# Performance work log

Measured on AMD Instinct MI355X. Metric: run time of the kernel, lower is better.

## Reference

```python
import jax, jax.numpy as jnp
import numpy as np

N_NODES = 50000
N_EDGES = 800000
HIDDEN = 128
HEADS = 8
HEAD_DIM = HIDDEN // HEADS
N_REL = 64
SCALE = np.sqrt(HEAD_DIM).astype(np.float32)


def setup_inputs() -> dict:
    key = jax.random.key(0)
    ks = jax.random.split(key, 12)
    s = 1.0 / np.sqrt(2 * HIDDEN)
    s2 = 1.0 / np.sqrt(HIDDEN)
    return {
        "node_features": jax.random.normal(ks[0], (N_NODES, HIDDEN), jnp.float32),
        "query_embedding": jax.random.normal(ks[1], (1, HIDDEN), jnp.float32),
        "relation_embeddings": jax.random.normal(ks[2], (N_REL, HIDDEN), jnp.float32),
        "Wq": jax.random.uniform(ks[3], (2 * HIDDEN, HIDDEN), jnp.float32, -s, s),
        "bq": jnp.zeros((HIDDEN,), jnp.float32),
        "Wk": jax.random.uniform(ks[4], (2 * HIDDEN, HIDDEN), jnp.float32, -s, s),
        "bk": jnp.zeros((HIDDEN,), jnp.float32),
        "Wv": jax.random.uniform(ks[5], (HIDDEN, HIDDEN), jnp.float32, -s2, s2),
        "bv": jnp.zeros((HIDDEN,), jnp.float32),
        "Wo": jax.random.uniform(ks[6], (HIDDEN, HIDDEN), jnp.float32, -s2, s2),
        "bo": jnp.zeros((HIDDEN,), jnp.float32),
        "edge_index": jax.random.randint(ks[7], (2, N_EDGES), 0, N_NODES, jnp.int64),
        "edge_type": jax.random.randint(ks[8], (N_EDGES,), 0, N_REL, jnp.int64),
    }


def reference(node_features, query_embedding, relation_embeddings,
              Wq, bq, Wk, bk, Wv, bv, Wo, bo, edge_index, edge_type):
    n = node_features.shape[0]
    # expand query to all nodes and concat: [N, 2*hidden]
    q_exp = jnp.broadcast_to(query_embedding, (n, HIDDEN))
    nq = jnp.concatenate([node_features, q_exp], axis=-1)
    q = (nq @ Wq + bq).reshape(n, HEADS, HEAD_DIM)
    k = (nq @ Wk + bk).reshape(n, HEADS, HEAD_DIM)
    v = (node_features @ Wv + bv).reshape(n, HEADS, HEAD_DIM)

    src, dst = edge_index[0], edge_index[1]
    rel_bias = relation_embeddings[edge_type].reshape(-1, HEADS, HEAD_DIM)

    # edge-wise scores [E, heads]
    scores = jnp.sum(q[dst] * (k[src] + rel_bias), axis=-1) / SCALE

    # sparse softmax grouped by dst; torch init of max buffer is 0 -> clamp at 0
    seg_max = jax.ops.segment_max(scores, dst, num_segments=n)
    seg_max = jnp.maximum(seg_max, 0.0)
    exp_s = jnp.exp(scores - seg_max[dst])
    seg_sum = jax.ops.segment_sum(exp_s, dst, num_segments=n)
    attn = exp_s / (seg_sum[dst] + 1e-8)  # [E, heads]

    messages = attn[:, :, None] * v[src]  # [E, heads, head_dim]
    out = jax.ops.segment_sum(messages, dst, num_segments=n)  # [N, heads, head_dim]
    out = out.reshape(n, HIDDEN)
    return out @ Wo + bo
```

## Files before the change

### kernel.cpp

```cpp
#include <hip/hip_runtime.h>
#include <math.h>

#define N_NODES 50000
#define N_EDGES 800000
#define HID 128
#define HEADS 8
#define HDIM 16
#define NBIN 196
#define CAPB 5120
#define K2_BLOCKS 196
#define K2_EPT 16
#define QKV_BLOCKS 782
#define NFB_BLOCKS 3125

typedef __attribute__((ext_vector_type(8))) short short8;
typedef __attribute__((ext_vector_type(4))) float floatx4;

#if defined(__has_builtin)
#if __has_builtin(__builtin_amdgcn_fdot2_f32_bf16)
#define HAVE_DOT2 1
#endif
#endif
#ifndef HAVE_DOT2
#define HAVE_DOT2 0
#endif

#if HAVE_DOT2
typedef __attribute__((ext_vector_type(2))) __bf16 bf16x2;
__device__ __forceinline__ float dot2acc(unsigned int a, unsigned int b, float c) {
    return __builtin_amdgcn_fdot2_f32_bf16(__builtin_bit_cast(bf16x2, a),
                                           __builtin_bit_cast(bf16x2, b), c, false);
}
#endif

__device__ __forceinline__ float bf_lo(unsigned int d) { return __uint_as_float(d << 16); }
__device__ __forceinline__ float bf_hi(unsigned int d) { return __uint_as_float(d & 0xFFFF0000u); }
__device__ __forceinline__ unsigned short f2bf(float f) {
    unsigned int u = __float_as_uint(f);
    u = (u + 0x7FFFu + ((u >> 16) & 1u)) >> 16;
    return (unsigned short)u;
}
__device__ __forceinline__ unsigned int pack_bf2(float a, float b) {
    return (unsigned int)f2bf(a) | ((unsigned int)f2bf(b) << 16);
}

__global__ __launch_bounds__(256) void prep_kernel(
    const float* __restrict__ nf,
    const float* __restrict__ query, const float* __restrict__ rel,
    const float* __restrict__ Wq, const float* __restrict__ bq,
    const float* __restrict__ Wk, const float* __restrict__ bk,
    const float* __restrict__ Wv, const float* __restrict__ Wo,
    const int* __restrict__ ei, const int* __restrict__ et,
    int* __restrict__ cursor, unsigned long long* __restrict__ recs,
    unsigned short* __restrict__ Wt, unsigned short* __restrict__ relbf,
    float* __restrict__ bqe, float* __restrict__ bke,
    unsigned short* __restrict__ nfb) {
    int b = blockIdx.x, tid = threadIdx.x;
    if (b < K2_BLOCKS) {
        __shared__ int hist[NBIN];
        __shared__ int base2[NBIN];
        __shared__ int lcur[NBIN];
        for (int i = tid; i < NBIN; i += 256) { hist[i] = 0; lcur[i] = 0; }
        __syncthreads();
        int e0 = b * (256 * K2_EPT);
        unsigned long long rec[K2_EPT];
        int bin[K2_EPT];
        #pragma unroll
        for (int i = 0; i < K2_EPT; ++i) {
            int e = e0 + i * 256 + tid;
            bin[i] = -1;
            if (e < N_EDGES) {
                unsigned int d = (unsigned)ei[N_EDGES + e];
                unsigned int s = (unsigned)ei[e];
                unsigned int t = (unsigned)et[e];
                rec[i] = ((unsigned long long)d << 22) | (t << 16) | s;
                bin[i] = (int)(d >> 8);
                atomicAdd(&hist[bin[i]], 1);
            }
        }
        __syncthreads();
        for (int i = tid; i < NBIN; i += 256) {
            int c = hist[i];
            base2[i] = (c > 0) ? (i * CAPB + atomicAdd(&cursor[i], c)) : 0;
        }
        __syncthreads();
        #pragma unroll
        for (int i = 0; i < K2_EPT; ++i) {
            if (bin[i] >= 0) {
                int pos = atomicAdd(&lcur[bin[i]], 1);
                recs[(size_t)base2[bin[i]] + pos] = rec[i];
            }
        }
        return;
    }
    b -= K2_BLOCKS;
    if (b < NFB_BLOCKS) {
        int base = b * 2048 + tid * 8;
        const float4* p = (const float4*)(nf + base);
        float4 a0 = p[0], a1 = p[1];
        short8 f;
        f[0] = (short)f2bf(a0.x); f[1] = (short)f2bf(a0.y);
        f[2] = (short)f2bf(a0.z); f[3] = (short)f2bf(a0.w);
        f[4] = (short)f2bf(a1.x); f[5] = (short)f2bf(a1.y);
        f[6] = (short)f2bf(a1.z); f[7] = (short)f2bf(a1.w);
        *(short8*)(nfb + base) = f;
        return;
    }
    b -= NFB_BLOCKS;
    if (b < 256) {
        int idx = b * 256 + tid;
        if (idx < 64 * HID) relbf[idx] = f2bf(rel[idx]);
        int m = idx >> 14;
        int rem = idx & 16383;
        int n = rem >> 7, k = rem & 127;
        const float* W = (m == 0) ? Wq : (m == 1) ? Wk : (m == 2) ? Wv : Wo;
        Wt[idx] = f2bf(W[k * HID + n]);
        return;
    }
    {
        __shared__ float fred[256];
        const float* W  = (b == 256) ? Wq : Wk;
        const float* bb = (b == 256) ? bq : bk;
        float* dst      = (b == 256) ? bqe : bke;
        int j = tid & 127;
        int half = tid >> 7;
        float a = 0.0f;
        int i0 = half * 64;
        for (int i = 0; i < 64; ++i) a += query[i0 + i] * W[(HID + i0 + i) * HID + j];
        fred[tid] = a;
        __syncthreads();
        if (half == 0) dst[j] = fred[j] + fred[128 + j] + bb[j];
    }
}

__global__ __launch_bounds__(256) void qkv_kernel(
    const unsigned short* __restrict__ nfb, const unsigned short* __restrict__ Wt,
    const float* __restrict__ bqe, const float* __restrict__ bke, const float* __restrict__ bv,
    const int* __restrict__ cursor, const unsigned long long* __restrict__ recs,
    unsigned int* __restrict__ esort, unsigned int* __restrict__ nodeinfo,
    unsigned short* __restrict__ qb16, unsigned short* __restrict__ kv16) {
    if (blockIdx.x < NBIN) {
        int bkt = blockIdx.x;
        int tid = threadIdx.x;
        __shared__ int hist[256];
        __shared__ int scan[256];
        __shared__ int sbase[256];
        __shared__ int lcur[256];
        hist[tid] = 0; lcur[tid] = 0;
        __syncthreads();
        int cnt = cursor[bkt];
        const unsigned long long* rb = recs + (size_t)bkt * CAPB;
        for (int i = tid; i < cnt; i += 256)
            atomicAdd(&hist[(int)((rb[i] >> 22) & 0xFF)], 1);
        __syncthreads();
        int v = hist[tid];
        scan[tid] = v;
        __syncthreads();
        for (int off = 1; off < 256; off <<= 1) {
            int a = (tid >= off) ? scan[tid - off] : 0;
            __syncthreads();
            scan[tid] += a;
            __syncthreads();
        }
        int excl = scan[tid] - v;
        sbase[tid] = excl;
        int node = bkt * 256 + tid;
        if (node < N_NODES) {
            unsigned int startg = (unsigned)(bkt * CAPB + excl);
            unsigned int deg = (unsigned)(v < 255 ? v : 255);
            nodeinfo[node] = (startg << 8) | deg;
        }
        __syncthreads();
        for (int i = tid; i < cnt; i += 256) {
            unsigned long long r = rb[i];
            int low = (int)((r >> 22) & 0xFF);
            int pos = atomicAdd(&lcur[low], 1);
            esort[(size_t)bkt * CAPB + sbase[low] + pos] = (unsigned int)(r & 0x3FFFFF);
        }
        return;
    }
    int row0 = (blockIdx.x - NBIN) * 64;
    int wave = threadIdx.x >> 6;
    int lane = threadIdx.x & 63;
    int col  = lane & 15;
    int quad = lane >> 4;

    short8 afr[4][4];
    #pragma unroll
    for (int t = 0; t < 4; ++t) {
        int arow = row0 + t * 16 + col;
        int asafe = (arow < N_NODES) ? arow : (N_NODES - 1);
        #pragma unroll
        for (int kk = 0; kk < 4; ++kk)
            afr[t][kk] = *(const short8*)(nfb + (size_t)asafe * HID + kk * 32 + quad * 8);
    }
    const float* biases[3] = {bqe, bke, bv};
    #pragma unroll
    for (int m = 0; m < 3; ++m) {
        const unsigned short* W = Wt + (size_t)m * HID * HID;
        #pragma unroll
        for (int nn = 0; nn < 2; ++nn) {
            int n = wave * 2 + nn;
            float b = biases[m][n * 16 + col];
            floatx4 acc[4];
            #pragma unroll
            for (int t = 0; t < 4; ++t) acc[t] = (floatx4){b, b, b, b};
            short8 bfr[4];
            #pragma unroll
            for (int kk = 0; kk < 4; ++kk)
                bfr[kk] = *(const short8*)(W + (size_t)(n * 16 + col) * HID + kk * 32 + quad * 8);
            #pragma unroll
            for (int kk = 0; kk < 4; ++kk)
                #pragma unroll
                for (int t = 0; t < 4; ++t)
                    acc[t] = __builtin_amdgcn_mfma_f32_16x16x32_bf16(afr[t][kk], bfr[kk], acc[t], 0, 0, 0);
            #pragma unroll
            for (int t = 0; t < 4; ++t) {
                #pragma unroll
                for (int i = 0; i < 4; ++i) {
                    int r = row0 + t * 16 + quad * 4 + i;
                    if (r < N_NODES) {
                        int c = n * 16 + col;
                        if (m == 0)      qb16[(size_t)r * HID + c] = f2bf(acc[t][i]);
                        else if (m == 1) kv16[(size_t)r * 256 + c] = f2bf(acc[t][i]);
                        else             kv16[(size_t)r * 256 + 128 + c] = f2bf(acc[t][i]);
                    }
                }
            }
        }
    }
}

__global__ __launch_bounds__(256) void attn_kernel(
    const unsigned int* __restrict__ qb, const unsigned int* __restrict__ kvu,
    const unsigned int* __restrict__ relu,
    const unsigned int* __restrict__ nodeinfo, const unsigned int* __restrict__ esort,
    unsigned int* __restrict__ abuf) {
    int node = blockIdx.x * 4 + (threadIdx.x >> 6);
    int lane = threadIdx.x & 63;
    int h = lane & 7;
    int hd = lane >> 3;
    int qi = lane & 15;
    int quarter = lane >> 4;
    unsigned int info = nodeinfo[node];
    int deg = (int)(info & 0xFF);
    unsigned int start = info >> 8;

    const uint4* qp = (const uint4*)(qb + (unsigned)node * 64 + h * 8);
    uint4 qa = qp[0], qc = qp[1];
#if !HAVE_DOT2
    float qf0 = bf_lo(qa.x), qf1 = bf_hi(qa.x), qf2 = bf_lo(qa.y), qf3 = bf_hi(qa.y);
    float qf4 = bf_lo(qa.z), qf5 = bf_hi(qa.z), qf6 = bf_lo(qa.w), qf7 = bf_hi(qa.w);
    float qf8 = bf_lo(qc.x), qf9 = bf_hi(qc.x), qf10 = bf_lo(qc.y), qf11 = bf_hi(qc.y);
    float qf12 = bf_lo(qc.z), qf13 = bf_hi(qc.z), qf14 = bf_lo(qc.w), qf15 = bf_hi(qc.w);
#endif

    float ssum = 0.0f;
    float acc[8] = {0.f, 0.f, 0.f, 0.f, 0.f, 0.f, 0.f, 0.f};
    for (int base = 0; base < deg; base += 16) {
        int el0 = base + hd;
        int el1 = el0 + 8;
        unsigned int pk0 = esort[start + ((el0 < deg) ? el0 : 0)];
        unsigned int pk1 = esort[start + ((el1 < deg) ? el1 : 0)];
        unsigned int src0 = pk0 & 0xFFFF, etv0 = (pk0 >> 16) & 0x3F;
        unsigned int src1 = pk1 & 0xFFFF, etv1 = (pk1 >> 16) & 0x3F;
        const uint4* kp0 = (const uint4*)(kvu + (src0 << 7) + h * 8);
        const uint4* rp0 = (const uint4*)(relu + (etv0 << 6) + h * 8);
        const uint4* kp1 = (const uint4*)(kvu + (src1 << 7) + h * 8);
        const uint4* rp1 = (const uint4*)(relu + (etv1 << 6) + h * 8);
        uint4 ka0 = kp0[0], kb0 = kp0[1];
        uint4 ra0 = rp0[0], rb0 = rp0[1];
        uint4 ka1 = kp1[0], kb1 = kp1[1];
        uint4 ra1 = rp1[0], rb1 = rp1[1];
        float s0, s1;
#if HAVE_DOT2
        {
            float a0 = dot2acc(qa.x, ka0.x, 0.0f), a1 = dot2acc(qa.y, ka0.y, 0.0f);
            float a2 = dot2acc(qa.z, ka0.z, 0.0f), a3 = dot2acc(qa.w, ka0.w, 0.0f);
            a0 = dot2acc(qc.x, kb0.x, a0); a1 = dot2acc(qc.y, kb0.y, a1);
            a2 = dot2acc(qc.z, kb0.z, a2); a3 = dot2acc(qc.w, kb0.w, a3);
            a0 = dot2acc(qa.x, ra0.x, a0); a1 = dot2acc(qa.y, ra0.y, a1);
            a2 = dot2acc(qa.z, ra0.z, a2); a3 = dot2acc(qa.w, ra0.w, a3);
            a0 = dot2acc(qc.x, rb0.x, a0); a1 = dot2acc(qc.y, rb0.y, a1);
            a2 = dot2acc(qc.z, rb0.z, a2); a3 = dot2acc(qc.w, rb0.w, a3);
            s0 = (a0 + a1) + (a2 + a3);
        }
        {
            float a0 = dot2acc(qa.x, ka1.x, 0.0f), a1 = dot2acc(qa.y, ka1.y, 0.0f);
            float a2 = dot2acc(qa.z, ka1.z, 0.0f), a3 = dot2acc(qa.w, ka1.w, 0.0f);
            a0 = dot2acc(qc.x, kb1.x, a0); a1 = dot2acc(qc.y, kb1.y, a1);
            a2 = dot2acc(qc.z, kb1.z, a2); a3 = dot2acc(qc.w, kb1.w, a3);
            a0 = dot2acc(qa.x, ra1.x, a0); a1 = dot2acc(qa.y, ra1.y, a1);
            a2 = dot2acc(qa.z, ra1.z, a2); a3 = dot2acc(qa.w, ra1.w, a3);
            a0 = dot2acc(qc.x, rb1.x, a0); a1 = dot2acc(qc.y, rb1.y, a1);
            a2 = dot2acc(qc.z, rb1.z, a2); a3 = dot2acc(qc.w, rb1.w, a3);
            s1 = (a0 + a1) + (a2 + a3);
        }
#else
        {
            float a0 = qf0 * (bf_lo(ka0.x) + bf_lo(ra0.x)) + qf4 * (bf_lo(ka0.z) + bf_lo(ra0.z))
                     + qf8 * (bf_lo(kb0.x) + bf_lo(rb0.x)) + qf12 * (bf_lo(kb0.z) + bf_lo(rb0.z));
            float a1 = qf1 * (bf_hi(ka0.x) + bf_hi(ra0.x)) + qf5 * (bf_hi(ka0.z) + bf_hi(ra0.z))
                     + qf9 * (bf_hi(kb0.x) + bf_hi(rb0.x)) + qf13 * (bf_hi(kb0.z) + bf_hi(rb0.z));
            float a2 = qf2 * (bf_lo(ka0.y) + bf_lo(ra0.y)) + qf6 * (bf_lo(ka0.w) + bf_lo(ra0.w))
                     + qf10 * (bf_lo(kb0.y) + bf_lo(rb0.y)) + qf14 * (bf_lo(kb0.w) + bf_lo(rb0.w));
            float a3 = qf3 * (bf_hi(ka0.y) + bf_hi(ra0.y)) + qf7 * (bf_hi(ka0.w) + bf_hi(ra0.w))
                     + qf11 * (bf_hi(kb0.y) + bf_hi(rb0.y)) + qf15 * (bf_hi(kb0.w) + bf_hi(rb0.w));
            s0 = (a0 + a1) + (a2 + a3);
        }
        {
            float a0 = qf0 * (bf_lo(ka1.x) + bf_lo(ra1.x)) + qf4 * (bf_lo(ka1.z) + bf_lo(ra1.z))
                     + qf8 * (bf_lo(kb1.x) + bf_lo(rb1.x)) + qf12 * (bf_lo(kb1.z) + bf_lo(rb1.z));
            float a1 = qf1 * (bf_hi(ka1.x) + bf_hi(ra1.x)) + qf5 * (bf_hi(ka1.z) + bf_hi(ra1.z))
                     + qf9 * (bf_hi(kb1.x) + bf_hi(rb1.x)) + qf13 * (bf_hi(kb1.z) + bf_hi(rb1.z));
            float a2 = qf2 * (bf_lo(ka1.y) + bf_lo(ra1.y)) + qf6 * (bf_lo(ka1.w) + bf_lo(ra1.w))
                     + qf10 * (bf_lo(kb1.y) + bf_lo(rb1.y)) + qf14 * (bf_lo(kb1.w) + bf_lo(rb1.w));
            float a3 = qf3 * (bf_hi(ka1.y) + bf_hi(ra1.y)) + qf7 * (bf_hi(ka1.w) + bf_hi(ra1.w))
                     + qf11 * (bf_hi(kb1.y) + bf_hi(rb1.y)) + qf15 * (bf_hi(kb1.w) + bf_hi(rb1.w));
            s1 = (a0 + a1) + (a2 + a3);
        }
#endif
        unsigned int wb0 = (el0 < deg) ? (unsigned int)f2bf(__expf(s0 * 0.25f)) : 0u;
        unsigned int wb1 = (el1 < deg) ? (unsigned int)f2bf(__expf(s1 * 0.25f)) : 0u;
        ssum += __uint_as_float(wb0 << 16) + __uint_as_float(wb1 << 16);
        unsigned int pw0 = (wb0 << 16) | src0;
        unsigned int pw1 = (wb1 << 16) | src1;
        #pragma unroll
        for (int t = 0; t < 4; ++t) {
            unsigned int pj = (t < 2) ? __shfl(pw0, (t * 4 + quarter) * 8 + (qi >> 1))
                                      : __shfl(pw1, ((t - 2) * 4 + quarter) * 8 + (qi >> 1));
            float wj = bf_hi(pj);
            unsigned int sj = pj & 0xFFFFu;
            uint4 v = *(const uint4*)(kvu + (sj << 7) + 64 + qi * 4);
            acc[0] += wj * bf_lo(v.x); acc[1] += wj * bf_hi(v.x);
            acc[2] += wj * bf_lo(v.y); acc[3] += wj * bf_hi(v.y);
            acc[4] += wj * bf_lo(v.z); acc[5] += wj * bf_hi(v.z);
            acc[6] += wj * bf_lo(v.w); acc[7] += wj * bf_hi(v.w);
        }
    }
    #pragma unroll
    for (int off = 8; off < 64; off <<= 1) ssum += __shfl_xor(ssum, off);
    #pragma unroll
    for (int k = 0; k < 8; ++k) {
        acc[k] += __shfl_xor(acc[k], 16);
        acc[k] += __shfl_xor(acc[k], 32);
    }
    float inv = 1.0f / (__shfl(ssum, qi >> 1) + 1e-8f);
    if (lane < 16) {
        uint4 o;
        o.x = pack_bf2(acc[0] * inv, acc[1] * inv);
        o.y = pack_bf2(acc[2] * inv, acc[3] * inv);
        o.z = pack_bf2(acc[4] * inv, acc[5] * inv);
        o.w = pack_bf2(acc[6] * inv, acc[7] * inv);
        *(uint4*)(abuf + (unsigned)node * 64 + qi * 4) = o;
    }
}

__global__ __launch_bounds__(256) void out_mfma_kernel(
    const unsigned short* __restrict__ abuf, const unsigned short* __restrict__ Wot,
    const float* __restrict__ bo, float* __restrict__ out) {
    int row0 = blockIdx.x * 64;
    int wave = threadIdx.x >> 6;
    int lane = threadIdx.x & 63;
    int col  = lane & 15;
    int quad = lane >> 4;

    short8 afr[4][4];
    #pragma unroll
    for (int t = 0; t < 4; ++t) {
        int arow = row0 + t * 16 + col;
        int asafe = (arow < N_NODES) ? arow : (N_NODES - 1);
        #pragma unroll
        for (int kk = 0; kk < 4; ++kk)
            afr[t][kk] = *(const short8*)(abuf + (size_t)asafe * HID + kk * 32 + quad * 8);
    }

    #pragma unroll
    for (int nn = 0; nn < 2; ++nn) {
        int n = wave * 2 + nn;
        float b = bo[n * 16 + col];
        floatx4 acc[4];
        #pragma unroll
        for (int t = 0; t < 4; ++t) acc[t] = (floatx4){b, b, b, b};
        short8 bfr[4];
        #pragma unroll
        for (int kk = 0; kk < 4; ++kk)
            bfr[kk] = *(const short8*)(Wot + (size_t)(n * 16 + col) * HID + kk * 32 + quad * 8);
        #pragma unroll
        for (int kk = 0; kk < 4; ++kk)
            #pragma unroll
            for (int t = 0; t < 4; ++t)
                acc[t] = __builtin_amdgcn_mfma_f32_16x16x32_bf16(afr[t][kk], bfr[kk], acc[t], 0, 0, 0);
        #pragma unroll
        for (int t = 0; t < 4; ++t) {
            #pragma unroll
            for (int i = 0; i < 4; ++i) {
                int r = row0 + t * 16 + quad * 4 + i;
                if (r < N_NODES) out[(size_t)r * HID + n * 16 + col] = acc[t][i];
            }
        }
    }
}

extern "C" void kernel_launch(void* const* d_in, const int* in_sizes, int n_in,
                              void* d_out, int out_size, void* d_ws, size_t ws_size,
                              hipStream_t stream) {
    const float* nf    = (const float*)d_in[0];
    const float* query = (const float*)d_in[1];
    const float* rel   = (const float*)d_in[2];
    const float* Wq    = (const float*)d_in[3];
    const float* bq    = (const float*)d_in[4];
    const float* Wk    = (const float*)d_in[5];
    const float* bk    = (const float*)d_in[6];
    const float* Wv    = (const float*)d_in[7];
    const float* bv    = (const float*)d_in[8];
    const float* Wo    = (const float*)d_in[9];
    const float* bo    = (const float*)d_in[10];
    const int*   ei    = (const int*)d_in[11];
    const int*   et    = (const int*)d_in[12];
    float* out = (float*)d_out;

    char* ws = (char*)d_ws;
    unsigned short* qb16 = (unsigned short*)ws; ws += (size_t)N_NODES * HID * 2;
    unsigned short* kv16 = (unsigned short*)ws; ws += (size_t)N_NODES * 256 * 2;
    unsigned int* abuf   = (unsigned int*)ws;   ws += (size_t)N_NODES * 64 * 4;
    float* bqe           = (float*)ws;          ws += 128 * 4;
    float* bke           = (float*)ws;          ws += 128 * 4;
    unsigned short* Wt   = (unsigned short*)ws; ws += (size_t)4 * HID * HID * 2;
    unsigned short* relbf = (unsigned short*)ws; ws += (size_t)64 * HID * 2;
    unsigned short* nfb  = (unsigned short*)ws; ws += (size_t)N_NODES * HID * 2;
    unsigned long long* recs = (unsigned long long*)ws; ws += (size_t)NBIN * CAPB * 8;
    unsigned int* esort  = (unsigned int*)ws;   ws += (size_t)NBIN * CAPB * 4;
    unsigned int* nodeinfo = (unsigned int*)ws; ws += (size_t)N_NODES * 4;
    int* cursor          = (int*)ws;            ws += (size_t)NBIN * 4;

    hipMemsetAsync(cursor, 0, (size_t)NBIN * 4, stream);
    prep_kernel<<<K2_BLOCKS + NFB_BLOCKS + 258, 256, 0, stream>>>(
        nf, query, rel, Wq, bq, Wk, bk, Wv, Wo, ei, et,
        cursor, recs, Wt, relbf, bqe, bke, nfb);
    qkv_kernel<<<NBIN + QKV_BLOCKS, 256, 0, stream>>>(
        nfb, Wt, bqe, bke, bv, cursor, recs, esort, nodeinfo, qb16, kv16);
    attn_kernel<<<N_NODES / 4, 256, 0, stream>>>(
        (const unsigned int*)qb16, (const unsigned int*)kv16,
        (const unsigned int*)relbf, nodeinfo, esort, abuf);
    out_mfma_kernel<<<QKV_BLOCKS, 256, 0, stream>>>(
        (const unsigned short*)abuf, Wt + (size_t)3 * HID * HID, bo, out);
}
```

Measured before the change: 213.5 us.

## Fuse attention with output projection and split QKV GEMM per matrix with LDS-staged stores

The attention kernel and the output projection are merged into one kernel. A 1024-thread block computes the attention rows for 64 nodes into an LDS tile, then runs the Wo MFMA from LDS, which removes the abuf round trip through global memory and one launch. The QKV GEMM is split into three times as many blocks, one weight matrix each, and stages results in LDS so global stores are coalesced 16-byte writes. The risks are lower parallelism in the fused kernel (782 large blocks, each wave handling 4 nodes serially), possible occupancy limits, and reloading the A fragments three times in the QKV stage.

New measurement: 247.5 us. 1.16x slower.

```diff
diff --git a/kernel.cpp b/kernel.cpp
--- a/kernel.cpp
+++ b/kernel.cpp
@@ -12,6 +12,7 @@
 #define K2_EPT 16
 #define QKV_BLOCKS 782
 #define NFB_BLOCKS 3125
+#define AO_BLOCKS 782
 
 typedef __attribute__((ext_vector_type(8))) short short8;
 typedef __attribute__((ext_vector_type(4))) float floatx4;
@@ -39,9 +40,6 @@
     unsigned int u = __float_as_uint(f);
     u = (u + 0x7FFFu + ((u >> 16) & 1u)) >> 16;
     return (unsigned short)u;
-}
-__device__ __forceinline__ unsigned int pack_bf2(float a, float b) {
-    return (unsigned int)f2bf(a) | ((unsigned int)f2bf(b) << 16);
 }
 
 __global__ __launch_bounds__(256) void prep_kernel(
@@ -179,11 +177,14 @@
         }
         return;
     }
-    int row0 = (blockIdx.x - NBIN) * 64;
+    int idx = blockIdx.x - NBIN;
+    int m = idx / QKV_BLOCKS;
+    int row0 = (idx - m * QKV_BLOCKS) * 64;
     int wave = threadIdx.x >> 6;
     int lane = threadIdx.x & 63;
     int col  = lane & 15;
     int quad = lane >> 4;
+    __shared__ unsigned short ctile[64][136];
 
     short8 afr[4][4];
     #pragma unroll
@@ -194,209 +195,201 @@
         for (int kk = 0; kk < 4; ++kk)
             afr[t][kk] = *(const short8*)(nfb + (size_t)asafe * HID + kk * 32 + quad * 8);
     }
-    const float* biases[3] = {bqe, bke, bv};
+    const float* bias = (m == 0) ? bqe : (m == 1) ? bke : bv;
+    const unsigned short* W = Wt + (size_t)m * HID * HID;
     #pragma unroll
-    for (int m = 0; m < 3; ++m) {
-        const unsigned short* W = Wt + (size_t)m * HID * HID;
-        #pragma unroll
-        for (int nn = 0; nn < 2; ++nn) {
-            int n = wave * 2 + nn;
-            float b = biases[m][n * 16 + col];
-            floatx4 acc[4];
-            #pragma unroll
-            for (int t = 0; t < 4; ++t) acc[t] = (floatx4){b, b, b, b};
-            short8 bfr[4];
-            #pragma unroll
-            for (int kk = 0; kk < 4; ++kk)
-                bfr[kk] = *(const short8*)(W + (size_t)(n * 16 + col) * HID + kk * 32 + quad * 8);
-            #pragma unroll
-            for (int kk = 0; kk < 4; ++kk)
-                #pragma unroll
-                for (int t = 0; t < 4; ++t)
-                    acc[t] = __builtin_amdgcn_mfma_f32_16x16x32_bf16(afr[t][kk], bfr[kk], acc[t], 0, 0, 0);
-            #pragma unroll
-            for (int t = 0; t < 4; ++t) {
-                #pragma unroll
-                for (int i = 0; i < 4; ++i) {
-                    int r = row0 + t * 16 + quad * 4 + i;
-                    if (r < N_NODES) {
-                        int c = n * 16 + col;
-                        if (m == 0)      qb16[(size_t)r * HID + c] = f2bf(acc[t][i]);
-                        else if (m == 1) kv16[(size_t)r * 256 + c] = f2bf(acc[t][i]);
-                        else             kv16[(size_t)r * 256 + 128 + c] = f2bf(acc[t][i]);
-                    }
-                }
-            }
-        }
-    }
-}
-
-__global__ __launch_bounds__(256) void attn_kernel(
+    for (int nn = 0; nn < 2; ++nn) {
+        int n = wave * 2 + nn;
+        float b = bias[n * 16 + col];
+        floatx4 acc[4];
+        #pragma unroll
+        for (int t = 0; t < 4; ++t) acc[t] = (floatx4){b, b, b, b};
+        short8 bfr[4];
+        #pragma unroll
+        for (int kk = 0; kk < 4; ++kk)
+            bfr[kk] = *(const short8*)(W + (size_t)(n * 16 + col) * HID + kk * 32 + quad * 8);
+        #pragma unroll
+        for (int kk = 0; kk < 4; ++kk)
+            #pragma unroll
+            for (int t = 0; t < 4; ++t)
+                acc[t] = __builtin_amdgcn_mfma_f32_16x16x32_bf16(afr[t][kk], bfr[kk], acc[t], 0, 0, 0);
+        #pragma unroll
+        for (int t = 0; t < 4; ++t)
+            #pragma unroll
+            for (int i = 0; i < 4; ++i)
+                ctile[t * 16 + quad * 4 + i][n * 16 + col] = f2bf(acc[t][i]);
+    }
+    __syncthreads();
+    #pragma unroll
+    for (int k = 0; k < 4; ++k) {
+        int chunk = threadIdx.x + k * 256;
+        int r = chunk >> 4, c = chunk & 15;
+        int row = row0 + r;
+        if (row < N_NODES) {
+            uint4 v = *(const uint4*)&ctile[r][c * 8];
+            unsigned short* dst = (m == 0) ? (qb16 + (size_t)row * HID + c * 8)
+                                           : (kv16 + (size_t)row * 256 + (m == 2 ? 128 : 0) + c * 8);
+            *(uint4*)dst = v;
+        }
+    }
+}
+
+__global__ __launch_bounds__(1024, 8) void attn_out_kernel(
     const unsigned int* __restrict__ qb, const unsigned int* __restrict__ kvu,
     const unsigned int* __restrict__ relu,
     const unsigned int* __restrict__ nodeinfo, const unsigned int* __restrict__ esort,
-    unsigned int* __restrict__ abuf) {
-    int node = blockIdx.x * 4 + (threadIdx.x >> 6);
+    const unsigned short* __restrict__ Wot, const float* __restrict__ bo,
+    float* __restrict__ out) {
+    __shared__ unsigned short atile[64][136];
+    int wave = threadIdx.x >> 6;
     int lane = threadIdx.x & 63;
     int h = lane & 7;
     int hd = lane >> 3;
     int qi = lane & 15;
     int quarter = lane >> 4;
-    unsigned int info = nodeinfo[node];
-    int deg = (int)(info & 0xFF);
-    unsigned int start = info >> 8;
-
-    const uint4* qp = (const uint4*)(qb + (unsigned)node * 64 + h * 8);
-    uint4 qa = qp[0], qc = qp[1];
+    int row0 = blockIdx.x * 64;
+
+    for (int rep = 0; rep < 4; ++rep) {
+        int r = wave * 4 + rep;
+        int node = row0 + r;
+        int nodeS = (node < N_NODES) ? node : (N_NODES - 1);
+        unsigned int info = nodeinfo[nodeS];
+        int deg = (node < N_NODES) ? (int)(info & 0xFF) : 0;
+        unsigned int start = info >> 8;
+
+        const uint4* qp = (const uint4*)(qb + (unsigned)nodeS * 64 + h * 8);
+        uint4 qa = qp[0], qc = qp[1];
 #if !HAVE_DOT2
-    float qf0 = bf_lo(qa.x), qf1 = bf_hi(qa.x), qf2 = bf_lo(qa.y), qf3 = bf_hi(qa.y);
-    float qf4 = bf_lo(qa.z), qf5 = bf_hi(qa.z), qf6 = bf_lo(qa.w), qf7 = bf_hi(qa.w);
-    float qf8 = bf_lo(qc.x), qf9 = bf_hi(qc.x), qf10 = bf_lo(qc.y), qf11 = bf_hi(qc.y);
-    float qf12 = bf_lo(qc.z), qf13 = bf_hi(qc.z), qf14 = bf_lo(qc.w), qf15 = bf_hi(qc.w);
-#endif
-
-    float ssum = 0.0f;
-    float acc[8] = {0.f, 0.f, 0.f, 0.f, 0.f, 0.f, 0.f, 0.f};
-    for (int base = 0; base < deg; base += 16) {
-        int el0 = base + hd;
-        int el1 = el0 + 8;
-        unsigned int pk0 = esort[start + ((el0 < deg) ? el0 : 0)];
-        unsigned int pk1 = esort[start + ((el1 < deg) ? el1 : 0)];
-        unsigned int src0 = pk0 & 0xFFFF, etv0 = (pk0 >> 16) & 0x3F;
-        unsigned int src1 = pk1 & 0xFFFF, etv1 = (pk1 >> 16) & 0x3F;
-        const uint4* kp0 = (const uint4*)(kvu + (src0 << 7) + h * 8);
-        const uint4* rp0 = (const uint4*)(relu + (etv0 << 6) + h * 8);
-        const uint4* kp1 = (const uint4*)(kvu + (src1 << 7) + h * 8);
-        const uint4* rp1 = (const uint4*)(relu + (etv1 << 6) + h * 8);
-        uint4 ka0 = kp0[0], kb0 = kp0[1];
-        uint4 ra0 = rp0[0], rb0 = rp0[1];
-        uint4 ka1 = kp1[0], kb1 = kp1[1];
-        uint4 ra1 = rp1[0], rb1 = rp1[1];
-        float s0, s1;
+        float qf0 = bf_lo(qa.x), qf1 = bf_hi(qa.x), qf2 = bf_lo(qa.y), qf3 = bf_hi(qa.y);
+        float qf4 = bf_lo(qa.z), qf5 = bf_hi(qa.z), qf6 = bf_lo(qa.w), qf7 = bf_hi(qa.w);
+        float qf8 = bf_lo(qc.x), qf9 = bf_hi(qc.x), qf10 = bf_lo(qc.y), qf11 = bf_hi(qc.y);
+        float qf12 = bf_lo(qc.z), qf13 = bf_hi(qc.z), qf14 = bf_lo(qc.w), qf15 = bf_hi(qc.w);
+#endif
+        float ssum = 0.0f;
+        float acc[8] = {0.f, 0.f, 0.f, 0.f, 0.f, 0.f, 0.f, 0.f};
+        for (int base = 0; base < deg; base += 16) {
+            int el0 = base + hd;
+            int el1 = el0 + 8;
+            unsigned int pk0 = esort[start + ((el0 < deg) ? el0 : 0)];
+            unsigned int pk1 = esort[start + ((el1 < deg) ? el1 : 0)];
+            unsigned int src0 = pk0 & 0xFFFF, etv0 = (pk0 >> 16) & 0x3F;
+            unsigned int src1 = pk1 & 0xFFFF, etv1 = (pk1 >> 16) & 0x3F;
+            const uint4* kp0 = (const uint4*)(kvu + (src0 << 7) + h * 8);
+            const uint4* rp0 = (const uint4*)(relu + (etv0 << 6) + h * 8);
+            const uint4* kp1 = (const uint4*)(kvu + (src1 << 7) + h * 8);
+            const uint4* rp1 = (const uint4*)(relu + (etv1 << 6) + h * 8);
+            uint4 ka0 = kp0[0], kb0 = kp0[1];
+            uint4 ra0 = rp0[0], rb0 = rp0[1];
+            uint4 ka1 = kp1[0], kb1 = kp1[1];
+            uint4 ra1 = rp1[0], rb1 = rp1[1];
+            float s0, s1;
 #if HAVE_DOT2
-        {
-            float a0 = dot2acc(qa.x, ka0.x, 0.0f), a1 = dot2acc(qa.y, ka0.y, 0.0f);
-            float a2 = dot2acc(qa.z, ka0.z, 0.0f), a3 = dot2acc(qa.w, ka0.w, 0.0f);
-            a0 = dot2acc(qc.x, kb0.x, a0); a1 = dot2acc(qc.y, kb0.y, a1);
-            a2 = dot2acc(qc.z, kb0.z, a2); a3 = dot2acc(qc.w, kb0.w, a3);
-            a0 = dot2acc(qa.x, ra0.x, a0); a1 = dot2acc(qa.y, ra0.y, a1);
-            a2 = dot2acc(qa.z, ra0.z, a2); a3 = dot2acc(qa.w, ra0.w, a3);
-            a0 = dot2acc(qc.x, rb0.x, a0); a1 = dot2acc(qc.y, rb0.y, a1);
-            a2 = dot2acc(qc.z, rb0.z, a2); a3 = dot2acc(qc.w, rb0.w, a3);
-            s0 = (a0 + a1) + (a2 + a3);
-        }
-        {
-            float a0 = dot2acc(qa.x, ka1.x, 0.0f), a1 = dot2acc(qa.y, ka1.y, 0.0f);
-            float a2 = dot2acc(qa.z, ka1.z, 0.0f), a3 = dot2acc(qa.w, ka1.w, 0.0f);
-            a0 = dot2acc(qc.x, kb1.x, a0); a1 = dot2acc(qc.y, kb1.y, a1);
-            a2 = dot2acc(qc.z, kb1.z, a2); a3 = dot2acc(qc.w, kb1.w, a3);
-            a0 = dot2acc(qa.x, ra1.x, a0); a1 = dot2acc(qa.y, ra1.y, a1);
-            a2 = dot2acc(qa.z, ra1.z, a2); a3 = dot2acc(qa.w, ra1.w, a3);
-            a0 = dot2acc(qc.x, rb1.x, a0); a1 = dot2acc(qc.y, rb1.y, a1);
-            a2 = dot2acc(qc.z, rb1.z, a2); a3 = dot2acc(qc.w, rb1.w, a3);
-            s1 = (a0 + a1) + (a2 + a3);
-        }
+            {
+                float a0 = dot2acc(qa.x, ka0.x, 0.0f), a1 = dot2acc(qa.y, ka0.y, 0.0f);
+                float a2 = dot2acc(qa.z, ka0.z, 0.0f), a3 = dot2acc(qa.w, ka0.w, 0.0f);
+                a0 = dot2acc(qc.x, kb0.x, a0); a1 = dot2acc(qc.y, kb0.y, a1);
+                a2 = dot2acc(qc.z, kb0.z, a2); a3 = dot2acc(qc.w, kb0.w, a3);
+                a0 = dot2acc(qa.x, ra0.x, a0); a1 = dot2acc(qa.y, ra0.y, a1);
+                a2 = dot2acc(qa.z, ra0.z, a2); a3 = dot2acc(qa.w, ra0.w, a3);
+                a0 = dot2acc(qc.x, rb0.x, a0); a1 = dot2acc(qc.y, rb0.y, a1);
+                a2 = dot2acc(qc.z, rb0.z, a2); a3 = dot2acc(qc.w, rb0.w, a3);
+                s0 = (a0 + a1) + (a2 + a3);
+            }
+            {
+                float a0 = dot2acc(qa.x, ka1.x, 0.0f), a1 = dot2acc(qa.y, ka1.y, 0.0f);
+                float a2 = dot2acc(qa.z, ka1.z, 0.0f), a3 = dot2acc(qa.w, ka1.w, 0.0f);
+                a0 = dot2acc(qc.x, kb1.x, a0); a1 = dot2acc(qc.y, kb1.y, a1);
+                a2 = dot2acc(qc.z, kb1.z, a2); a3 = dot2acc(qc.w, kb1.w, a3);
+                a0 = dot2acc(qa.x, ra1.x, a0); a1 = dot2acc(qa.y, ra1.y, a1);
+                a2 = dot2acc(qa.z, ra1.z, a2); a3 = dot2acc(qa.w, ra1.w, a3);
+                a0 = dot2acc(qc.x, rb1.x, a0); a1 = dot2acc(qc.y, rb1.y, a1);
+                a2 = dot2acc(qc.z, rb1.z, a2); a3 = dot2acc(qc.w, rb1.w, a3);
+                s1 = (a0 + a1) + (a2 + a3);
+            }
 #else
-        {
-            float a0 = qf0 * (bf_lo(ka0.x) + bf_lo(ra0.x)) + qf4 * (bf_lo(ka0.z) + bf_lo(ra0.z))
-                     + qf8 * (bf_lo(kb0.x) + bf_lo(rb0.x)) + qf12 * (bf_lo(kb0.z) + bf_lo(rb0.z));
-            float a1 = qf1 * (bf_hi(ka0.x) + bf_hi(ra0.x)) + qf5 * (bf_hi(ka0.z) + bf_hi(ra0.z))
-                     + qf9 * (bf_hi(kb0.x) + bf_hi(rb0.x)) + qf13 * (bf_hi(kb0.z) + bf_hi(rb0.z));
-            float a2 = qf2 * (bf_lo(ka0.y) + bf_lo(ra0.y)) + qf6 * (bf_lo(ka0.w) + bf_lo(ra0.w))
-                     + qf10 * (bf_lo(kb0.y) + bf_lo(rb0.y)) + qf14 * (bf_lo(kb0.w) + bf_lo(rb0.w));
-            float a3 = qf3 * (bf_hi(ka0.y) + bf_hi(ra0.y)) + qf7 * (bf_hi(ka0.w) + bf_hi(ra0.w))
-                     + qf11 * (bf_hi(kb0.y) + bf_hi(rb0.y)) + qf15 * (bf_hi(kb0.w) + bf_hi(rb0.w));
-            s0 = (a0 + a1) + (a2 + a3);
-        }
-        {
-            float a0 = qf0 * (bf_lo(ka1.x) + bf_lo(ra1.x)) + qf4 * (bf_lo(ka1.z) + bf_lo(ra1.z))
-                     + qf8 * (bf_lo(kb1.x) + bf_lo(rb1.x)) + qf12 * (bf_lo(kb1.z) + bf_lo(rb1.z));
-            float a1 = qf1 * (bf_hi(ka1.x) + bf_hi(ra1.x)) + qf5 * (bf_hi(ka1.z) + bf_hi(ra1.z))
-                     + qf9 * (bf_hi(kb1.x) + bf_hi(rb1.x)) + qf13 * (bf_hi(kb1.z) + bf_hi(rb1.z));
-            float a2 = qf2 * (bf_lo(ka1.y) + bf_lo(ra1.y)) + qf6 * (bf_lo(ka1.w) + bf_lo(ra1.w))
-                     + qf10 * (bf_lo(kb1.y) + bf_lo(rb1.y)) + qf14 * (bf_lo(kb1.w) + bf_lo(rb1.w));
-            float a3 = qf3 * (bf_hi(ka1.y) + bf_hi(ra1.y)) + qf7 * (bf_hi(ka1.w) + bf_hi(ra1.w))
-                     + qf11 * (bf_hi(kb1.y) + bf_hi(rb1.y)) + qf15 * (bf_hi(kb1.w) + bf_hi(rb1.w));
-            s1 = (a0 + a1) + (a2 + a3);
-        }
-#endif
-        unsigned int wb0 = (el0 < deg) ? (unsigned int)f2bf(__expf(s0 * 0.25f)) : 0u;
-        unsigned int wb1 = (el1 < deg) ? (unsigned int)f2bf(__expf(s1 * 0.25f)) : 0u;
-        ssum += __uint_as_float(wb0 << 16) + __uint_as_float(wb1 << 16);
-        unsigned int pw0 = (wb0 << 16) | src0;
-        unsigned int pw1 = (wb1 << 16) | src1;
-        #pragma unroll
-        for (int t = 0; t < 4; ++t) {
-            unsigned int pj = (t < 2) ? __shfl(pw0, (t * 4 + quarter) * 8 + (qi >> 1))
-                                      : __shfl(pw1, ((t - 2) * 4 + quarter) * 8 + (qi >> 1));
-            float wj = bf_hi(pj);
-            unsigned int sj = pj & 0xFFFFu;
-            uint4 v = *(const uint4*)(kvu + (sj << 7) + 64 + qi * 4);
-            acc[0] += wj * bf_lo(v.x); acc[1] += wj * bf_hi(v.x);
-            acc[2] += wj * bf_lo(v.y); acc[3] += wj * bf_hi(v.y);
-            acc[4] += wj * bf_lo(v.z); acc[5] += wj * bf_hi(v.z);
-            acc[6] += wj * bf_lo(v.w); acc[7] += wj * bf_hi(v.w);
-        }
-    }
-    #pragma unroll
-    for (int off = 8; off < 64; off <<= 1) ssum += __shfl_xor(ssum, off);
-    #pragma unroll
-    for (int k = 0; k < 8; ++k) {
-        acc[k] += __shfl_xor(acc[k], 16);
-        acc[k] += __shfl_xor(acc[k], 32);
-    }
-    float inv = 1.0f / (__shfl(ssum, qi >> 1) + 1e-8f);
-    if (lane < 16) {
-        uint4 o;
-        o.x = pack_bf2(acc[0] * inv, acc[1] * inv);
-        o.y = pack_bf2(acc[2] * inv, acc[3] * inv);
-        o.z = pack_bf2(acc[4] * inv, acc[5] * inv);
-        o.w = pack_bf2(acc[6] * inv, acc[7] * inv);
-        *(uint4*)(abuf + (unsigned)node * 64 + qi * 4) = o;
-    }
-}
-
-__global__ __launch_bounds__(256) void out_mfma_kernel(
-    const unsigned short* __restrict__ abuf, const unsigned short* __restrict__ Wot,
-    const float* __restrict__ bo, float* __restrict__ out) {
-    int row0 = blockIdx.x * 64;
-    int wave = threadIdx.x >> 6;
-    int lane = threadIdx.x & 63;
-    int col  = lane & 15;
-    int quad = lane >> 4;
-
-    short8 afr[4][4];
-    #pragma unroll
-    for (int t = 0; t < 4; ++t) {
-        int arow = row0 + t * 16 + col;
-        int asafe = (arow < N_NODES) ? arow : (N_NODES - 1);
-        #pragma unroll
-        for (int kk = 0; kk < 4; ++kk)
-            afr[t][kk] = *(const short8*)(abuf + (size_t)asafe * HID + kk * 32 + quad * 8);
-    }
-
-    #pragma unroll
-    for (int nn = 0; nn < 2; ++nn) {
-        int n = wave * 2 + nn;
+            {
+                float a0 = qf0 * (bf_lo(ka0.x) + bf_lo(ra0.x)) + qf4 * (bf_lo(ka0.z) + bf_lo(ra0.z))
+                         + qf8 * (bf_lo(kb0.x) + bf_lo(rb0.x)) + qf12 * (bf_lo(kb0.z) + bf_lo(rb0.z));
+                float a1 = qf1 * (bf_hi(ka0.x) + bf_hi(ra0.x)) + qf5 * (bf_hi(ka0.z) + bf_hi(ra0.z))
+                         + qf9 * (bf_hi(kb0.x) + bf_hi(rb0.x)) + qf13 * (bf_hi(kb0.z) + bf_hi(rb0.z));
+                float a2 = qf2 * (bf_lo(ka0.y) + bf_lo(ra0.y)) + qf6 * (bf_lo(ka0.w) + bf_lo(ra0.w))
+                         + qf10 * (bf_lo(kb0.y) + bf_lo(rb0.y)) + qf14 * (bf_lo(kb0.w) + bf_lo(rb0.w));
+                float a3 = qf3 * (bf_hi(ka0.y) + bf_hi(ra0.y)) + qf7 * (bf_hi(ka0.w) + bf_hi(ra0.w))
+                         + qf11 * (bf_hi(kb0.y) + bf_hi(rb0.y)) + qf15 * (bf_hi(kb0.w) + bf_hi(rb0.w));
+                s0 = (a0 + a1) + (a2 + a3);
+            }
+            {
+                float a0 = qf0 * (bf_lo(ka1.x) + bf_lo(ra1.x)) + qf4 * (bf_lo(ka1.z) + bf_lo(ra1.z))
+                         + qf8 * (bf_lo(kb1.x) + bf_lo(rb1.x)) + qf12 * (bf_lo(kb1.z) + bf_lo(rb1.z));
+                float a1 = qf1 * (bf_hi(ka1.x) + bf_hi(ra1.x)) + qf5 * (bf_hi(ka1.z) + bf_hi(ra1.z))
+                         + qf9 * (bf_hi(kb1.x) + bf_hi(rb1.x)) + qf13 * (bf_hi(kb1.z) + bf_hi(rb1.z));
+                float a2 = qf2 * (bf_lo(ka1.y) + bf_lo(ra1.y)) + qf6 * (bf_lo(ka1.w) + bf_lo(ra1.w))
+                         + qf10 * (bf_lo(kb1.y) + bf_lo(rb1.y)) + qf14 * (bf_lo(kb1.w) + bf_lo(rb1.w));
+                float a3 = qf3 * (bf_hi(ka1.y) + bf_hi(ra1.y)) + qf7 * (bf_hi(ka1.w) + bf_hi(ra1.w))
+                         + qf11 * (bf_hi(kb1.y) + bf_hi(rb1.y)) + qf15 * (bf_hi(kb1.w) + bf_hi(rb1.w));
+                s1 = (a0 + a1) + (a2 + a3);
+            }
+#endif
+            unsigned int wb0 = (el0 < deg) ? (unsigned int)f2bf(__expf(s0 * 0.25f)) : 0u;
+            unsigned int wb1 = (el1 < deg) ? (unsigned int)f2bf(__expf(s1 * 0.25f)) : 0u;
+            ssum += __uint_as_float(wb0 << 16) + __uint_as_float(wb1 << 16);
+            unsigned int pw0 = (wb0 << 16) | src0;
+            unsigned int pw1 = (wb1 << 16) | src1;
+            #pragma unroll
+            for (int t = 0; t < 4; ++t) {
+                unsigned int pj = (t < 2) ? __shfl(pw0, (t * 4 + quarter) * 8 + (qi >> 1))
+                                          : __shfl(pw1, ((t - 2) * 4 + quarter) * 8 + (qi >> 1));
+                float wj = bf_hi(pj);
+                unsigned int sj = pj & 0xFFFFu;
+                uint4 v = *(const uint4*)(kvu + (sj << 7) + 64 + qi * 4);
+                acc[0] += wj * bf_lo(v.x); acc[1] += wj * bf_hi(v.x);
+                acc[2] += wj * bf_lo(v.y); acc[3] += wj * bf_hi(v.y);
+                acc[4] += wj * bf_lo(v.z); acc[5] += wj * bf_hi(v.z);
+                acc[6] += wj * bf_lo(v.w); acc[7] += wj * bf_hi(v.w);
+            }
+        }
+        #pragma unroll
+        for (int off = 8; off < 64; off <<= 1) ssum += __shfl_xor(ssum, off);
+        #pragma unroll
+        for (int k = 0; k < 8; ++k) {
+            acc[k] += __shfl_xor(acc[k], 16);
+            acc[k] += __shfl_xor(acc[k], 32);
+        }
+        float inv = 1.0f / (__shfl(ssum, qi >> 1) + 1e-8f);
+        if (lane < 16) {
+            short8 o;
+            #pragma unroll
+            for (int k = 0; k < 8; ++k) o[k] = (short)f2bf(acc[k] * inv);
+            *(short8*)&atile[r][qi * 8] = o;
+        }
+    }
+    __syncthreads();
+    if (wave < 8) {
+        int n = wave;
+        int col = lane & 15;
+        int quad = lane >> 4;
         float b = bo[n * 16 + col];
-        floatx4 acc[4];
-        #pragma unroll
-        for (int t = 0; t < 4; ++t) acc[t] = (floatx4){b, b, b, b};
         short8 bfr[4];
         #pragma unroll
         for (int kk = 0; kk < 4; ++kk)
             bfr[kk] = *(const short8*)(Wot + (size_t)(n * 16 + col) * HID + kk * 32 + quad * 8);
-        #pragma unroll
-        for (int kk = 0; kk < 4; ++kk)
-            #pragma unroll
-            for (int t = 0; t < 4; ++t)
-                acc[t] = __builtin_amdgcn_mfma_f32_16x16x32_bf16(afr[t][kk], bfr[kk], acc[t], 0, 0, 0);
+        floatx4 oacc[4];
+        #pragma unroll
+        for (int t = 0; t < 4; ++t) oacc[t] = (floatx4){b, b, b, b};
+        #pragma unroll
+        for (int kk = 0; kk < 4; ++kk) {
+            #pragma unroll
+            for (int t = 0; t < 4; ++t) {
+                short8 a = *(const short8*)&atile[t * 16 + col][kk * 32 + quad * 8];
+                oacc[t] = __builtin_amdgcn_mfma_f32_16x16x32_bf16(a, bfr[kk], oacc[t], 0, 0, 0);
+            }
+        }
         #pragma unroll
         for (int t = 0; t < 4; ++t) {
             #pragma unroll
             for (int i = 0; i < 4; ++i) {
                 int r = row0 + t * 16 + quad * 4 + i;
-                if (r < N_NODES) out[(size_t)r * HID + n * 16 + col] = acc[t][i];
+                if (r < N_NODES) out[(size_t)r * HID + n * 16 + col] = oacc[t][i];
             }
         }
     }
@@ -423,7 +416,6 @@
     char* ws = (char*)d_ws;
     unsigned short* qb16 = (unsigned short*)ws; ws += (size_t)N_NODES * HID * 2;
     unsigned short* kv16 = (unsigned short*)ws; ws += (size_t)N_NODES * 256 * 2;
-    unsigned int* abuf   = (unsigned int*)ws;   ws += (size_t)N_NODES * 64 * 4;
     float* bqe           = (float*)ws;          ws += 128 * 4;
     float* bke           = (float*)ws;          ws += 128 * 4;
     unsigned short* Wt   = (unsigned short*)ws; ws += (size_t)4 * HID * HID * 2;
@@ -438,11 +430,10 @@
     prep_kernel<<<K2_BLOCKS + NFB_BLOCKS + 258, 256, 0, stream>>>(
         nf, query, rel, Wq, bq, Wk, bk, Wv, Wo, ei, et,
         cursor, recs, Wt, relbf, bqe, bke, nfb);
-    qkv_kernel<<<NBIN + QKV_BLOCKS, 256, 0, stream>>>(
+    qkv_kernel<<<NBIN + 3 * QKV_BLOCKS, 256, 0, stream>>>(
         nfb, Wt, bqe, bke, bv, cursor, recs, esort, nodeinfo, qb16, kv16);
-    attn_kernel<<<N_NODES / 4, 256, 0, stream>>>(
+    attn_out_kernel<<<AO_BLOCKS, 1024, 0, stream>>>(
         (const unsigned int*)qb16, (const unsigned int*)kv16,
-        (const unsigned int*)relbf, nodeinfo, esort, abuf);
-    out_mfma_kernel<<<QKV_BLOCKS, 256, 0, stream>>>(
-        (const unsigned short*)abuf, Wt + (size_t)3 * HID * HID, bo, out);
-}
+        (const unsigned int*)relbf, nodeinfo, esort,
+        Wt + (size_t)3 * HID * HID, bo, out);
+}
```

## Split QKV projection across blocks, stage GEMM outputs in LDS for coalesced stores

Applied to the files above, without the earlier changes.

The QKV GEMM blocks are split three ways so each block computes only one of Q, K or V, tripling the block count for more parallelism. Both the QKV and output GEMMs now write their MFMA results into a padded shared-memory tile and then store full rows with 16-byte vector writes, replacing scattered 2- and 4-byte stores. The edge-binning part of prep gets four times more blocks, each handling fewer edges. In exchange, every QKV block reloads the node-feature A fragments for its projection, and both GEMMs add LDS usage and a barrier.

Result: slower. 225.1 us (+5.4%).

```diff
diff --git a/kernel.cpp b/kernel.cpp
--- a/kernel.cpp
+++ b/kernel.cpp
@@ -8,8 +8,8 @@
 #define HDIM 16
 #define NBIN 196
 #define CAPB 5120
-#define K2_BLOCKS 196
-#define K2_EPT 16
+#define K2_BLOCKS 784
+#define K2_EPT 4
 #define QKV_BLOCKS 782
 #define NFB_BLOCKS 3125
 
@@ -179,11 +179,14 @@
         }
         return;
     }
-    int row0 = (blockIdx.x - NBIN) * 64;
+    int idx = blockIdx.x - NBIN;
+    int m = idx / QKV_BLOCKS;
+    int row0 = (idx - m * QKV_BLOCKS) * 64;
     int wave = threadIdx.x >> 6;
     int lane = threadIdx.x & 63;
     int col  = lane & 15;
     int quad = lane >> 4;
+    __shared__ unsigned short ctile[64][136];
 
     short8 afr[4][4];
     #pragma unroll
@@ -194,39 +197,41 @@
         for (int kk = 0; kk < 4; ++kk)
             afr[t][kk] = *(const short8*)(nfb + (size_t)asafe * HID + kk * 32 + quad * 8);
     }
-    const float* biases[3] = {bqe, bke, bv};
-    #pragma unroll
-    for (int m = 0; m < 3; ++m) {
-        const unsigned short* W = Wt + (size_t)m * HID * HID;
-        #pragma unroll
-        for (int nn = 0; nn < 2; ++nn) {
-            int n = wave * 2 + nn;
-            float b = biases[m][n * 16 + col];
-            floatx4 acc[4];
+    const float* bias = (m == 0) ? bqe : (m == 1) ? bke : bv;
+    const unsigned short* W = Wt + (size_t)m * HID * HID;
+    #pragma unroll
+    for (int nn = 0; nn < 2; ++nn) {
+        int n = wave * 2 + nn;
+        float b = bias[n * 16 + col];
+        floatx4 acc[4];
+        #pragma unroll
+        for (int t = 0; t < 4; ++t) acc[t] = (floatx4){b, b, b, b};
+        short8 bfr[4];
+        #pragma unroll
+        for (int kk = 0; kk < 4; ++kk)
+            bfr[kk] = *(const short8*)(W + (size_t)(n * 16 + col) * HID + kk * 32 + quad * 8);
+        #pragma unroll
+        for (int kk = 0; kk < 4; ++kk)
             #pragma unroll
-            for (int t = 0; t < 4; ++t) acc[t] = (floatx4){b, b, b, b};
-            short8 bfr[4];
+            for (int t = 0; t < 4; ++t)
+                acc[t] = __builtin_amdgcn_mfma_f32_16x16x32_bf16(afr[t][kk], bfr[kk], acc[t], 0, 0, 0);
+        #pragma unroll
+        for (int t = 0; t < 4; ++t)
             #pragma unroll
-            for (int kk = 0; kk < 4; ++kk)
-                bfr[kk] = *(const short8*)(W + (size_t)(n * 16 + col) * HID + kk * 32 + quad * 8);
-            #pragma unroll
-            for (int kk = 0; kk < 4; ++kk)
-                #pragma unroll
-                for (int t = 0; t < 4; ++t)
-                    acc[t] = __builtin_amdgcn_mfma_f32_16x16x32_bf16(afr[t][kk], bfr[kk], acc[t], 0, 0, 0);
-            #pragma unroll
-            for (int t = 0; t < 4; ++t) {
-                #pragma unroll
-                for (int i = 0; i < 4; ++i) {
-                    int r = row0 + t * 16 + quad * 4 + i;
-                    if (r < N_NODES) {
-                        int c = n * 16 + col;
-                        if (m == 0)      qb16[(size_t)r * HID + c] = f2bf(acc[t][i]);
-                        else if (m == 1) kv16[(size_t)r * 256 + c] = f2bf(acc[t][i]);
-                        else             kv16[(size_t)r * 256 + 128 + c] = f2bf(acc[t][i]);
-                    }
-                }
-            }
+            for (int i = 0; i < 4; ++i)
+                ctile[t * 16 + quad * 4 + i][n * 16 + col] = f2bf(acc[t][i]);
+    }
+    __syncthreads();
+    #pragma unroll
+    for (int k = 0; k < 4; ++k) {
+        int chunk = threadIdx.x + k * 256;
+        int r = chunk >> 4, c = chunk & 15;
+        int row = row0 + r;
+        if (row < N_NODES) {
+            uint4 v = *(const uint4*)&ctile[r][c * 8];
+            unsigned short* dst = (m == 0) ? (qb16 + (size_t)row * HID + c * 8)
+                                           : (kv16 + (size_t)row * 256 + (m == 2 ? 128 : 0) + c * 8);
+            *(uint4*)dst = v;
         }
     }
 }
@@ -364,6 +369,7 @@
     int lane = threadIdx.x & 63;
     int col  = lane & 15;
     int quad = lane >> 4;
+    __shared__ float otile[64][132];
 
     short8 afr[4][4];
     #pragma unroll
@@ -392,12 +398,20 @@
             for (int t = 0; t < 4; ++t)
                 acc[t] = __builtin_amdgcn_mfma_f32_16x16x32_bf16(afr[t][kk], bfr[kk], acc[t], 0, 0, 0);
         #pragma unroll
-        for (int t = 0; t < 4; ++t) {
+        for (int t = 0; t < 4; ++t)
             #pragma unroll
-            for (int i = 0; i < 4; ++i) {
-                int r = row0 + t * 16 + quad * 4 + i;
-                if (r < N_NODES) out[(size_t)r * HID + n * 16 + col] = acc[t][i];
-            }
+            for (int i = 0; i < 4; ++i)
+                otile[t * 16 + quad * 4 + i][n * 16 + col] = acc[t][i];
+    }
+    __syncthreads();
+    #pragma unroll
+    for (int k = 0; k < 8; ++k) {
+        int chunk = threadIdx.x + k * 256;
+        int r = chunk >> 5, c = chunk & 31;
+        int row = row0 + r;
+        if (row < N_NODES) {
+            float4 v = *(const float4*)&otile[r][c * 4];
+            *(float4*)(out + (size_t)row * HID + c * 4) = v;
         }
     }
 }
@@ -438,7 +452,7 @@
     prep_kernel<<<K2_BLOCKS + NFB_BLOCKS + 258, 256, 0, stream>>>(
         nf, query, rel, Wq, bq, Wk, bk, Wv, Wo, ei, et,
         cursor, recs, Wt, relbf, bqe, bke, nfb);
-    qkv_kernel<<<NBIN + QKV_BLOCKS, 256, 0, stream>>>(
+    qkv_kernel<<<NBIN + 3 * QKV_BLOCKS, 256, 0, stream>>>(
         nfb, Wt, bqe, bke, bv, cursor, recs, esort, nodeinfo, qb16, kv16);
     attn_kernel<<<N_NODES / 4, 256, 0, stream>>>(
         (const unsigned int*)qb16, (const unsigned int*)kv16,
```
